# Kernel tuning notes

Measured on AMD Instinct MI355X. Metric: run time of the kernel, lower is better.

The kernel has to match this reference:

```python
import jax, jax.numpy as jnp
import numpy as np

ALPHA = 8.3  # depth-similarity sharpness from the Depth-aware CNN paper
K = 3        # kernel size
PAD = 1      # padding (stride=1, dilation=1)


def setup_inputs() -> dict:
    key = jax.random.key(0)
    k1, k2, k3, k4 = jax.random.split(key, 4)
    B, Cin, Cout, H, W = 8, 128, 128, 128, 128
    inp = {
        "input": jax.random.normal(k1, (B, Cin, H, W), dtype=jnp.float32),
        "depth": jax.random.uniform(k2, (B, 1, H, W), dtype=jnp.float32),
        "weight": jax.random.normal(k3, (Cout, Cin, K, K), dtype=jnp.float32) * 0.05,
        "bias": jax.random.normal(k4, (Cout,), dtype=jnp.float32) * 0.05,
    }
    return inp


def reference(input, depth, weight, bias):
    # Depth-aware convolution: out(b,o,y,x) = sum_{c,kh,kw} W(o,c,kh,kw)
    #   * x(b,c,y+kh-1,x+kw-1) * exp(-ALPHA * |D(b,y,x) - D(b,y+kh-1,x+kw-1)|)
    # stride=1, dilation=1, padding=1 -> output spatial == input spatial.
    B, C, H, W = input.shape
    xp = jnp.pad(input, ((0, 0), (0, 0), (PAD, PAD), (PAD, PAD)))
    dp = jnp.pad(depth, ((0, 0), (0, 0), (PAD, PAD), (PAD, PAD)))
    acc = jnp.zeros((B, weight.shape[0], H, W), dtype=input.dtype)
    for kh in range(K):
        for kw in range(K):
            xs = xp[:, :, kh:kh + H, kw:kw + W]          # [B,C,H,W] shifted window
            ds = dp[:, :, kh:kh + H, kw:kw + W]          # [B,1,H,W]
            sim = jnp.exp(-ALPHA * jnp.abs(depth - ds))  # [B,1,H,W]
            acc = acc + jnp.einsum('bchw,oc->bohw', xs * sim, weight[:, :, kh, kw])
    return acc + bias[None, :, None, None]
```

## Files before the change

kernel.cpp:

```cpp
#include <hip/hip_runtime.h>
#include <hip/hip_bf16.h>
#include <cstdint>

#define ALPHA 8.3f

typedef __attribute__((ext_vector_type(8))) short bf16x8;
typedef __attribute__((ext_vector_type(4))) float f32x4;

__device__ __align__(16) short g_wt[9 * 128 * 128];

__device__ __forceinline__ short f2bf(float f) {
    union { float f; uint32_t u; } v; v.f = f;
    uint32_t r = v.u + 0x7fffu + ((v.u >> 16) & 1u);
    return (short)(r >> 16);
}

__global__ __launch_bounds__(256) void wt_transform(const float* __restrict__ w) {
    int tid = blockIdx.x * 256 + threadIdx.x;
    int c = tid & 127;
    int o = (tid >> 7) & 127;
    int tap = tid >> 14;
    g_wt[tid] = f2bf(w[(o * 128 + c) * 9 + tap]);
}

__global__ __launch_bounds__(256, 3) void depthconv_main(
    const float* __restrict__ x, const float* __restrict__ depth,
    const float* __restrict__ bias, float* __restrict__ out)
{
    __shared__ __align__(16) short Xs[3 * 66 * 128];
    __shared__ float simL[9][64];

    const int blk = blockIdx.x;
    const int b = blk >> 8;
    const int rem = blk & 255;
    const int h = rem >> 1;
    const int w0 = (rem & 1) << 6;

    const int tid = threadIdx.x;
    const int lane = tid & 63;
    const int wid = tid >> 6;

    const float* xb = x + (size_t)b * (128 * 128 * 128);
    const float* db = depth + (size_t)b * (128 * 128);
    char* xsp = (char*)Xs;

    for (int it = tid; it < 3168; it += 256) {
        int r = it / 1056;
        int rem2 = it - r * 1056;
        int oct = rem2 / 66;
        int wl = rem2 - oct * 66;
        int hh = h - 1 + r;
        int wg = w0 - 1 + wl;
        int row = r * 66 + wl;
        bf16x8 pk = (bf16x8){0, 0, 0, 0, 0, 0, 0, 0};
        if (hh >= 0 && hh < 128 && wg >= 0 && wg < 128) {
            const float* p = xb + (size_t)oct * 131072 + (size_t)hh * 128 + wg;
            #pragma unroll
            for (int i = 0; i < 8; ++i)
                pk[i] = f2bf(p[(size_t)i * 16384]);
        }
        int byte = ((row << 8) | (oct << 4)) ^ ((row & 15) << 4);
        *reinterpret_cast<bf16x8*>(xsp + byte) = pk;
    }

    for (int idx = tid; idx < 576; idx += 256) {
        int t = idx >> 6;
        int wo = idx & 63;
        int kh = t / 3, kw = t - 3 * kh;
        int w = w0 + wo;
        float dc = db[h * 128 + w];
        int hh = h + kh - 1, wg = w + kw - 1;
        float dsv = (hh >= 0 && hh < 128 && wg >= 0 && wg < 128)
                        ? db[hh * 128 + wg] : 0.f;
        simL[t][wo] = __expf(-ALPHA * fabsf(dc - dsv));
    }
    __syncthreads();

    f32x4 acc[2][4];
    #pragma unroll
    for (int i = 0; i < 2; ++i)
        #pragma unroll
        for (int j = 0; j < 4; ++j)
            acc[i][j] = (f32x4){0.f, 0.f, 0.f, 0.f};

    const int obase = wid << 5;
    const int l15 = lane & 15;
    const int khi = lane >> 4;

    for (int tap = 0; tap < 9; ++tap) {
        const int r = tap / 3;
        const int kw = tap - 3 * r;
        const short* wtap = g_wt + tap * 16384;

        f32x4 P[2][4];
        #pragma unroll
        for (int i = 0; i < 2; ++i)
            #pragma unroll
            for (int j = 0; j < 4; ++j)
                P[i][j] = (f32x4){0.f, 0.f, 0.f, 0.f};

        #pragma unroll
        for (int ks = 0; ks < 4; ++ks) {
            const int cb = ks * 32 + (khi << 3);
            bf16x8 afr[2], bfr[4];
            #pragma unroll
            for (int i = 0; i < 2; ++i) {
                int orow = obase + i * 16 + l15;
                afr[i] = *reinterpret_cast<const bf16x8*>(wtap + orow * 128 + cb);
            }
            #pragma unroll
            for (int j = 0; j < 4; ++j) {
                int wl = j * 16 + l15 + kw;
                int row = r * 66 + wl;
                int byte = ((row << 8) | (cb << 1)) ^ ((row & 15) << 4);
                bfr[j] = *reinterpret_cast<const bf16x8*>(xsp + byte);
            }
            #pragma unroll
            for (int i = 0; i < 2; ++i)
                #pragma unroll
                for (int j = 0; j < 4; ++j)
                    P[i][j] = __builtin_amdgcn_mfma_f32_16x16x32_bf16(
                        afr[i], bfr[j], P[i][j], 0, 0, 0);
        }

        #pragma unroll
        for (int j = 0; j < 4; ++j) {
            float sv = simL[tap][j * 16 + l15];
            #pragma unroll
            for (int i = 0; i < 2; ++i)
                #pragma unroll
                for (int rr = 0; rr < 4; ++rr)
                    acc[i][j][rr] += sv * P[i][j][rr];
        }
    }

    #pragma unroll
    for (int i = 0; i < 2; ++i) {
        #pragma unroll
        for (int rr = 0; rr < 4; ++rr) {
            const int o = obase + i * 16 + (khi << 2) + rr;
            const float bv = bias[o];
            float* orow = out + (((size_t)(b * 128 + o)) * 128 + h) * 128 + w0;
            #pragma unroll
            for (int j = 0; j < 4; ++j)
                orow[j * 16 + l15] = acc[i][j][rr] + bv;
        }
    }
}

extern "C" void kernel_launch(void* const* d_in, const int* in_sizes, int n_in,
                              void* d_out, int out_size, void* d_ws, size_t ws_size,
                              hipStream_t stream) {
    const float* x     = (const float*)d_in[0];
    const float* depth = (const float*)d_in[1];
    const float* wgt   = (const float*)d_in[2];
    const float* bias  = (const float*)d_in[3];
    float* out = (float*)d_out;

    hipLaunchKernelGGL(wt_transform, dim3(576), dim3(256), 0, stream, wgt);
    hipLaunchKernelGGL(depthconv_main, dim3(8 * 128 * 2), dim3(256), 0, stream,
                       x, depth, bias, out);
}
```

Before: 218.0 us.

## Pre-transpose input to padded NHWC bf16 and read MFMA operands from global

Adds a separate pass that converts the NCHW fp32 input into a zero-padded NHWC bf16 buffer, plus a padded depth buffer. The main kernel no longer stages a shared-memory tile or precomputes similarity tables. It reads B fragments and depth values straight from global memory and relies on the cache, which removes per-block gather, convert and barrier overhead. In exchange it adds an extra full read and write pass over the input and uncoalesced-style global fragment loads in the inner loop. It also drops the occupancy hint from the launch bounds.

```diff
diff --git a/kernel.cpp b/kernel.cpp
--- a/kernel.cpp
+++ b/kernel.cpp
@@ -8,6 +8,8 @@
 typedef __attribute__((ext_vector_type(4))) float f32x4;
 
 __device__ __align__(16) short g_wt[9 * 128 * 128];
+__device__ __align__(16) short g_xt[(size_t)8 * 130 * 130 * 128];
+__device__ float g_dp[8 * 130 * 130];
 
 __device__ __forceinline__ short f2bf(float f) {
     union { float f; uint32_t u; } v; v.f = f;
@@ -23,13 +25,51 @@
     g_wt[tid] = f2bf(w[(o * 128 + c) * 9 + tap]);
 }
 
-__global__ __launch_bounds__(256, 3) void depthconv_main(
-    const float* __restrict__ x, const float* __restrict__ depth,
+__global__ __launch_bounds__(256) void aux_fill(const float* __restrict__ depth) {
+    int idx = blockIdx.x * 256 + threadIdx.x;
+    if (idx < 135200) {
+        int b = idx / 16900;
+        int rem = idx - b * 16900;
+        int hp = rem / 130;
+        int wp = rem - hp * 130;
+        float v = 0.f;
+        if (hp >= 1 && hp <= 128 && wp >= 1 && wp <= 128)
+            v = depth[b * 16384 + (hp - 1) * 128 + (wp - 1)];
+        g_dp[idx] = v;
+    } else if (idx < 135200 + 66048) {
+        int u = idx - 135200;
+        int b = u / 8256;
+        int rem = u - b * 8256;
+        int pos = rem >> 4;
+        int unit = rem & 15;
+        int hp, wp;
+        if (pos < 130)      { hp = 0;           wp = pos; }
+        else if (pos < 260) { hp = 129;         wp = pos - 130; }
+        else if (pos < 388) { hp = pos - 259;   wp = 0; }
+        else                { hp = pos - 387;   wp = 129; }
+        size_t off = (((size_t)b * 130 + hp) * 130 + wp) * 128 + unit * 8;
+        *reinterpret_cast<bf16x8*>(g_xt + off) = (bf16x8){0,0,0,0,0,0,0,0};
+    }
+}
+
+__global__ __launch_bounds__(256) void x_transpose(const float* __restrict__ x) {
+    int g = blockIdx.x * 256 + threadIdx.x;
+    int oct = g & 15;
+    int w = (g >> 4) & 127;
+    int h = (g >> 11) & 127;
+    int b = g >> 18;
+    const float* p = x + ((size_t)(b * 128 + oct * 8)) * 16384 + h * 128 + w;
+    bf16x8 pk;
+    #pragma unroll
+    for (int i = 0; i < 8; ++i)
+        pk[i] = f2bf(p[(size_t)i * 16384]);
+    size_t off = (((size_t)b * 130 + h + 1) * 130 + w + 1) * 128 + oct * 8;
+    *reinterpret_cast<bf16x8*>(g_xt + off) = pk;
+}
+
+__global__ __launch_bounds__(256) void depthconv_main(
     const float* __restrict__ bias, float* __restrict__ out)
 {
-    __shared__ __align__(16) short Xs[3 * 66 * 128];
-    __shared__ float simL[9][64];
-
     const int blk = blockIdx.x;
     const int b = blk >> 8;
     const int rem = blk & 255;
@@ -39,42 +79,9 @@
     const int tid = threadIdx.x;
     const int lane = tid & 63;
     const int wid = tid >> 6;
-
-    const float* xb = x + (size_t)b * (128 * 128 * 128);
-    const float* db = depth + (size_t)b * (128 * 128);
-    char* xsp = (char*)Xs;
-
-    for (int it = tid; it < 3168; it += 256) {
-        int r = it / 1056;
-        int rem2 = it - r * 1056;
-        int oct = rem2 / 66;
-        int wl = rem2 - oct * 66;
-        int hh = h - 1 + r;
-        int wg = w0 - 1 + wl;
-        int row = r * 66 + wl;
-        bf16x8 pk = (bf16x8){0, 0, 0, 0, 0, 0, 0, 0};
-        if (hh >= 0 && hh < 128 && wg >= 0 && wg < 128) {
-            const float* p = xb + (size_t)oct * 131072 + (size_t)hh * 128 + wg;
-            #pragma unroll
-            for (int i = 0; i < 8; ++i)
-                pk[i] = f2bf(p[(size_t)i * 16384]);
-        }
-        int byte = ((row << 8) | (oct << 4)) ^ ((row & 15) << 4);
-        *reinterpret_cast<bf16x8*>(xsp + byte) = pk;
-    }
-
-    for (int idx = tid; idx < 576; idx += 256) {
-        int t = idx >> 6;
-        int wo = idx & 63;
-        int kh = t / 3, kw = t - 3 * kh;
-        int w = w0 + wo;
-        float dc = db[h * 128 + w];
-        int hh = h + kh - 1, wg = w + kw - 1;
-        float dsv = (hh >= 0 && hh < 128 && wg >= 0 && wg < 128)
-                        ? db[hh * 128 + wg] : 0.f;
-        simL[t][wo] = __expf(-ALPHA * fabsf(dc - dsv));
-    }
-    __syncthreads();
+    const int l15 = lane & 15;
+    const int khi = lane >> 4;
+    const int obase = wid << 5;
 
     f32x4 acc[2][4];
     #pragma unroll
@@ -83,54 +90,63 @@
         for (int j = 0; j < 4; ++j)
             acc[i][j] = (f32x4){0.f, 0.f, 0.f, 0.f};
 
-    const int obase = wid << 5;
-    const int l15 = lane & 15;
-    const int khi = lane >> 4;
+    const float* dpb = g_dp + b * 16900;
+    float dc[4];
+    #pragma unroll
+    for (int j = 0; j < 4; ++j)
+        dc[j] = dpb[(h + 1) * 130 + w0 + j * 16 + l15 + 1];
 
-    for (int tap = 0; tap < 9; ++tap) {
-        const int r = tap / 3;
-        const int kw = tap - 3 * r;
-        const short* wtap = g_wt + tap * 16384;
+    for (int r = 0; r < 3; ++r) {
+        #pragma unroll
+        for (int kw = 0; kw < 3; ++kw) {
+            const short* wtap = g_wt + (r * 3 + kw) * 16384;
+            const short* xrow = g_xt + (((size_t)b * 130 + h + r) * 130 + w0 + kw) * 128;
+            const float* drow = dpb + (h + r) * 130 + w0 + kw;
 
-        f32x4 P[2][4];
-        #pragma unroll
-        for (int i = 0; i < 2; ++i)
-            #pragma unroll
-            for (int j = 0; j < 4; ++j)
-                P[i][j] = (f32x4){0.f, 0.f, 0.f, 0.f};
-
-        #pragma unroll
-        for (int ks = 0; ks < 4; ++ks) {
-            const int cb = ks * 32 + (khi << 3);
-            bf16x8 afr[2], bfr[4];
-            #pragma unroll
-            for (int i = 0; i < 2; ++i) {
-                int orow = obase + i * 16 + l15;
-                afr[i] = *reinterpret_cast<const bf16x8*>(wtap + orow * 128 + cb);
-            }
+            float sim[4];
             #pragma unroll
             for (int j = 0; j < 4; ++j) {
-                int wl = j * 16 + l15 + kw;
-                int row = r * 66 + wl;
-                int byte = ((row << 8) | (cb << 1)) ^ ((row & 15) << 4);
-                bfr[j] = *reinterpret_cast<const bf16x8*>(xsp + byte);
+                float dsv = drow[j * 16 + l15];
+                sim[j] = __expf(-ALPHA * fabsf(dc[j] - dsv));
             }
+
+            f32x4 P[2][4];
             #pragma unroll
             for (int i = 0; i < 2; ++i)
                 #pragma unroll
                 for (int j = 0; j < 4; ++j)
-                    P[i][j] = __builtin_amdgcn_mfma_f32_16x16x32_bf16(
-                        afr[i], bfr[j], P[i][j], 0, 0, 0);
-        }
+                    P[i][j] = (f32x4){0.f, 0.f, 0.f, 0.f};
 
-        #pragma unroll
-        for (int j = 0; j < 4; ++j) {
-            float sv = simL[tap][j * 16 + l15];
             #pragma unroll
-            for (int i = 0; i < 2; ++i)
+            for (int ks = 0; ks < 4; ++ks) {
+                const int cb = ks * 32 + (khi << 3);
+                bf16x8 afr[2], bfr[4];
                 #pragma unroll
-                for (int rr = 0; rr < 4; ++rr)
-                    acc[i][j][rr] += sv * P[i][j][rr];
+                for (int i = 0; i < 2; ++i) {
+                    int orow = obase + i * 16 + l15;
+                    afr[i] = *reinterpret_cast<const bf16x8*>(wtap + orow * 128 + cb);
+                }
+                #pragma unroll
+                for (int j = 0; j < 4; ++j)
+                    bfr[j] = *reinterpret_cast<const bf16x8*>(
+                        xrow + (j * 16 + l15) * 128 + cb);
+                #pragma unroll
+                for (int i = 0; i < 2; ++i)
+                    #pragma unroll
+                    for (int j = 0; j < 4; ++j)
+                        P[i][j] = __builtin_amdgcn_mfma_f32_16x16x32_bf16(
+                            afr[i], bfr[j], P[i][j], 0, 0, 0);
+            }
+
+            #pragma unroll
+            for (int j = 0; j < 4; ++j) {
+                float sv = sim[j];
+                #pragma unroll
+                for (int i = 0; i < 2; ++i)
+                    #pragma unroll
+                    for (int rr = 0; rr < 4; ++rr)
+                        acc[i][j][rr] += sv * P[i][j][rr];
+            }
         }
     }
 
@@ -158,6 +174,8 @@
     float* out = (float*)d_out;
 
     hipLaunchKernelGGL(wt_transform, dim3(576), dim3(256), 0, stream, wgt);
+    hipLaunchKernelGGL(aux_fill, dim3(787), dim3(256), 0, stream, depth);
+    hipLaunchKernelGGL(x_transpose, dim3(8192), dim3(256), 0, stream, x);
     hipLaunchKernelGGL(depthconv_main, dim3(8 * 128 * 2), dim3(256), 0, stream,
-                       x, depth, bias, out);
+                       bias, out);
 }
```

Measured after the change: 366.5 us. +68.1%, slower.
